# Kernel tuning notes

Hardware: AMD Instinct MI355X
Metric: run time of the kernel (lower is better)

## Reference

```python
import jax, jax.numpy as jnp
import numpy as np

D_MODEL = 1024
N_HEADS = 16
HEAD_DIM = D_MODEL // N_HEADS


def setup_inputs() -> dict:
    key = jax.random.key(0)
    ks = jax.random.split(key, 5)
    s = 1.0 / np.sqrt(D_MODEL)
    return {
        "x": jax.random.normal(ks[0], (2, 2048, D_MODEL), dtype=jnp.float32),
        "w_qkv": jax.random.uniform(ks[1], (3 * D_MODEL, D_MODEL), jnp.float32, -s, s),
        "b_qkv": jax.random.uniform(ks[2], (3 * D_MODEL,), jnp.float32, -s, s),
        "w_out": jax.random.uniform(ks[3], (D_MODEL, D_MODEL), jnp.float32, -s, s),
        "b_out": jax.random.uniform(ks[4], (D_MODEL,), jnp.float32, -s, s),
    }


def _attn(x, w_qkv, b_qkv, w_out, b_out):
    bsz, seq_len, _ = x.shape
    qkv = jnp.einsum('bsd,ed->bse', x, w_qkv) + b_qkv  # [B,S,3D]
    q, k, v = jnp.split(qkv, 3, axis=-1)
    def heads(t):  # [B,S,D] -> [B,H,S,Dh]
        return t.reshape(bsz, seq_len, N_HEADS, HEAD_DIM).transpose(0, 2, 1, 3)
    q, k, v = heads(q), heads(k), heads(v)
    scores = jnp.einsum('bhqd,bhkd->bhqk', q, k) / np.sqrt(HEAD_DIM)
    mask = jnp.tril(jnp.ones((seq_len, seq_len), dtype=bool))
    scores = jnp.where(mask, scores, -jnp.inf)
    probs = jax.nn.softmax(scores, axis=-1)
    attn = jnp.einsum('bhqk,bhkd->bhqd', probs, v)
    attn = attn.transpose(0, 2, 1, 3).reshape(bsz, seq_len, D_MODEL)
    return jnp.einsum('bsd,ed->bse', attn, w_out) + b_out


def reference(x, w_qkv, b_qkv, w_out, b_out):
    return _attn(x, w_qkv, b_qkv, w_out, b_out)
```

## Files before the change

### kernel.cpp

```cpp
#include <hip/hip_runtime.h>
#include <hip/hip_bf16.h>
#include <stdint.h>

#define SEQ     2048
#define BATCH   2
#define NHEADS  16
#define HDIM    64
#define DMODEL  1024
#define N3      3072
#define D2      2048
#define MTOT    (BATCH*SEQ)

typedef __attribute__((ext_vector_type(4))) float f32x4;
typedef __attribute__((ext_vector_type(8))) short bf16x8;

static __device__ inline unsigned short f2bf(float f) {
    union { float f; unsigned u; } v; v.f = f;
    unsigned r = (v.u + 0x7fffu + ((v.u >> 16) & 1u)) >> 16;
    return (unsigned short)r;
}
static __device__ inline unsigned pk2bf(float a, float b) {
    union { __hip_bfloat162 h; unsigned u; } c;
    c.h = __float22bfloat162_rn(make_float2(a, b));
    return c.u;
}

#define GLDS(gp, lp) __builtin_amdgcn_global_load_lds( \
    (const __attribute__((address_space(1))) void*)(gp), \
    (__attribute__((address_space(3))) void*)(lp), 16, 0, 0)

__global__ void cast_all(const float* __restrict__ x,
                         const float* __restrict__ wqkv,
                         const float* __restrict__ wout,
                         unsigned short* __restrict__ xb,
                         unsigned short* __restrict__ wqkvb,
                         unsigned short* __restrict__ woutb) {
    long i4 = (long)(blockIdx.x * blockDim.x + threadIdx.x) * 4;
    const float* src; unsigned short* dst; long off;
    if (i4 < 4194304L)      { src = x;    dst = xb;    off = i4; }
    else if (i4 < 7340032L) { src = wqkv; dst = wqkvb; off = i4 - 4194304L; }
    else                    { src = wout; dst = woutb; off = i4 - 7340032L; }
    float4 v = *(const float4*)(src + off);
    union { uint2 u; ushort4 s; } pk;
    pk.u.x = pk2bf(v.x, v.y); pk.u.y = pk2bf(v.z, v.w);
    *(ushort4*)(dst + off) = pk.s;
}

__global__ __launch_bounds__(512, 1) void gemm_qkv(
    const unsigned short* __restrict__ A,
    const unsigned short* __restrict__ B,
    const float* __restrict__ bias,
    unsigned short* __restrict__ qk,
    unsigned short* __restrict__ vT)
{
    __shared__ __align__(16) unsigned short sA[2][256][64];
    __shared__ __align__(16) unsigned short sB[2][256][64];
    const int tid  = threadIdx.x;
    const int w    = tid >> 6, lane = tid & 63;
    const int quad = lane >> 4, l16 = lane & 15, l7 = l16 & 7;
    const int wm = w >> 2, wn = w & 3;
    const int bid = blockIdx.x;
    const int m0 = (bid & 15) << 8;
    const int n0 = (bid >> 4) << 8;

    f32x4 acc[8][4];
    const f32x4 zero = {0.f, 0.f, 0.f, 0.f};
    #pragma unroll
    for (int i = 0; i < 8; i++)
        #pragma unroll
        for (int j = 0; j < 4; j++) acc[i][j] = zero;

    const int rsel = tid >> 3;
    const int sgl  = (tid & 7) ^ (rsel & 7);
    const unsigned short* gA = A + (long)(m0 + rsel) * 1024 + sgl * 8;
    const unsigned short* gB = B + (long)(n0 + rsel) * 1024 + sgl * 8;

    #pragma unroll
    for (int j = 0; j < 4; j++) {
        GLDS(gA + (long)(64 * j) * 1024, &sA[0][64 * j + w * 8][0]);
        GLDS(gB + (long)(64 * j) * 1024, &sB[0][64 * j + w * 8][0]);
    }

    auto compute_tile = [&](const unsigned short (*A_)[64],
                            const unsigned short (*B_)[64]) {
        #pragma unroll
        for (int mh = 0; mh < 2; mh++) {
            bf16x8 af[4][2];
            #pragma unroll
            for (int mt2 = 0; mt2 < 4; mt2++)
                #pragma unroll
                for (int kk = 0; kk < 2; kk++)
                    af[mt2][kk] = *(const bf16x8*)(
                        &A_[wm * 128 + mh * 64 + mt2 * 16 + l16]
                           [(((kk << 2) + quad) ^ l7) * 8]);
            #pragma unroll
            for (int nh = 0; nh < 2; nh++) {
                bf16x8 bfr[2][2];
                #pragma unroll
                for (int nt2 = 0; nt2 < 2; nt2++)
                    #pragma unroll
                    for (int kk = 0; kk < 2; kk++)
                        bfr[nt2][kk] = *(const bf16x8*)(
                            &B_[wn * 64 + nh * 32 + nt2 * 16 + l16]
                               [(((kk << 2) + quad) ^ l7) * 8]);
                #pragma unroll
                for (int mt2 = 0; mt2 < 4; mt2++)
                    #pragma unroll
                    for (int nt2 = 0; nt2 < 2; nt2++)
                        #pragma unroll
                        for (int kk = 0; kk < 2; kk++)
                            acc[mh * 4 + mt2][nh * 2 + nt2] =
                                __builtin_amdgcn_mfma_f32_16x16x32_bf16(
                                    af[mt2][kk], bfr[nt2][kk],
                                    acc[mh * 4 + mt2][nh * 2 + nt2], 0, 0, 0);
            }
        }
    };

    for (int t = 0; t < 15; ++t) {
        const int nb = (t + 1) & 1, cb = t & 1;
        const long ko = (long)(t + 1) * 64;
        #pragma unroll
        for (int j = 0; j < 4; j++) {
            GLDS(gA + (long)(64 * j) * 1024 + ko, &sA[nb][64 * j + w * 8][0]);
            GLDS(gB + (long)(64 * j) * 1024 + ko, &sB[nb][64 * j + w * 8][0]);
        }
        __builtin_amdgcn_sched_barrier(0);
        asm volatile("s_waitcnt vmcnt(8)" ::: "memory");
        __builtin_amdgcn_sched_barrier(0);
        __builtin_amdgcn_s_barrier();
        compute_tile(sA[cb], sB[cb]);
        asm volatile("s_waitcnt lgkmcnt(0)" ::: "memory");
        __builtin_amdgcn_sched_barrier(0);
        __builtin_amdgcn_s_barrier();
    }
    asm volatile("s_waitcnt vmcnt(0)" ::: "memory");
    __builtin_amdgcn_sched_barrier(0);
    __builtin_amdgcn_s_barrier();
    compute_tile(sA[1], sB[1]);

    if (n0 < 2048) {
        #pragma unroll
        for (int nt = 0; nt < 4; nt++) {
            const int n_g = n0 + wn * 64 + nt * 16 + l16;
            const float bv = bias[n_g];
            #pragma unroll
            for (int mt = 0; mt < 8; mt++) {
                #pragma unroll
                for (int r = 0; r < 4; r++) {
                    const int m_g = m0 + wm * 128 + mt * 16 + quad * 4 + r;
                    qk[(long)m_g * D2 + n_g] = f2bf(acc[mt][nt][r] + bv);
                }
            }
        }
    } else {
        const int b = m0 >> 11;
        #pragma unroll
        for (int nt = 0; nt < 4; nt++) {
            const int n_g = n0 + wn * 64 + nt * 16 + l16;
            const int dm = n_g - 2048;
            const long vrow = (long)(((b << 4) + (dm >> 6)) << 6) + (dm & 63);
            const float bv = bias[n_g];
            #pragma unroll
            for (int mt = 0; mt < 8; mt++) {
                const int m_g = m0 + wm * 128 + mt * 16 + quad * 4;
                union { uint2 u; ushort4 s; } pk;
                pk.u.x = pk2bf(acc[mt][nt][0] + bv, acc[mt][nt][1] + bv);
                pk.u.y = pk2bf(acc[mt][nt][2] + bv, acc[mt][nt][3] + bv);
                *(ushort4*)(vT + vrow * D2 + (m_g & 2047)) = pk.s;
            }
        }
    }
}

__global__ __launch_bounds__(256, 2) void gemm_out(
    const unsigned short* __restrict__ A,
    const unsigned short* __restrict__ B,
    const float* __restrict__ bias,
    float* __restrict__ C)
{
    __shared__ __align__(16) unsigned short sA[2][128][64];
    __shared__ __align__(16) unsigned short sB[2][64][64];
    const int tid  = threadIdx.x;
    const int wave = tid >> 6, lane = tid & 63;
    const int quad = lane >> 4, l16 = lane & 15, l7 = l16 & 7;
    const int wm = wave >> 1, wn = wave & 1;
    const int m0 = blockIdx.x * 128, n0 = blockIdx.y * 64;

    f32x4 acc[4][2];
    const f32x4 zero = {0.f, 0.f, 0.f, 0.f};
    #pragma unroll
    for (int i = 0; i < 4; i++) { acc[i][0] = zero; acc[i][1] = zero; }

    const int rsel = tid >> 3;
    const int sgl  = (tid & 7) ^ (rsel & 7);
    const unsigned short* gA0 = A + (long)(m0 + rsel) * 1024 + sgl * 8;
    const unsigned short* gB0 = B + (long)(n0 + rsel) * 1024 + sgl * 8;

    #pragma unroll
    for (int i = 0; i < 4; i++)
        GLDS(gA0 + (long)(32 * i) * 1024, &sA[0][32 * i + wave * 8][0]);
    #pragma unroll
    for (int i = 0; i < 2; i++)
        GLDS(gB0 + (long)(32 * i) * 1024, &sB[0][32 * i + wave * 8][0]);

    int buf = 0;
    for (int k0 = 0; k0 < 1024; k0 += 64, buf ^= 1) {
        __syncthreads();
        if (k0 + 64 < 1024) {
            #pragma unroll
            for (int i = 0; i < 4; i++)
                GLDS(gA0 + (long)(32 * i) * 1024 + k0 + 64, &sA[buf ^ 1][32 * i + wave * 8][0]);
            #pragma unroll
            for (int i = 0; i < 2; i++)
                GLDS(gB0 + (long)(32 * i) * 1024 + k0 + 64, &sB[buf ^ 1][32 * i + wave * 8][0]);
        }
        #pragma unroll
        for (int ks = 0; ks < 2; ks++) {
            bf16x8 af[4], bfr[2];
            #pragma unroll
            for (int mt = 0; mt < 4; mt++)
                af[mt] = *(const bf16x8*)(&sA[buf][wm * 64 + mt * 16 + l16][((ks * 4 + quad) ^ l7) * 8]);
            #pragma unroll
            for (int nt = 0; nt < 2; nt++)
                bfr[nt] = *(const bf16x8*)(&sB[buf][wn * 32 + nt * 16 + l16][((ks * 4 + quad) ^ l7) * 8]);
            #pragma unroll
            for (int mt = 0; mt < 4; mt++)
                #pragma unroll
                for (int nt = 0; nt < 2; nt++)
                    acc[mt][nt] = __builtin_amdgcn_mfma_f32_16x16x32_bf16(
                        af[mt], bfr[nt], acc[mt][nt], 0, 0, 0);
        }
    }
    #pragma unroll
    for (int nt = 0; nt < 2; nt++) {
        const int n_g = n0 + wn * 32 + nt * 16 + l16;
        const float bv = bias[n_g];
        #pragma unroll
        for (int mt = 0; mt < 4; mt++) {
            #pragma unroll
            for (int r = 0; r < 4; r++) {
                const int m_g = m0 + wm * 64 + mt * 16 + quad * 4 + r;
                C[(long)m_g * DMODEL + n_g] = acc[mt][nt][r] + bv;
            }
        }
    }
}

__global__ __launch_bounds__(512, 1) void attn_kernel(
    const unsigned short* __restrict__ qk,
    const unsigned short* __restrict__ vT,
    unsigned short* __restrict__ attn)
{
    __shared__ __align__(16) unsigned short sK [2][2][64][64];
    __shared__ __align__(16) unsigned short sVt[2][2][64][64];
    __shared__ __align__(16) unsigned short sP [8][16][64];

    const int tid  = threadIdx.x;
    const int w    = tid >> 6, lane = tid & 63;
    const int quad = lane >> 4, l16 = lane & 15, l7 = l16 & 7;

    const int bh = blockIdx.x;
    const int b  = bh >> 4, h = bh & 15;
    const int pair = blockIdx.y;
    const long rowb = (long)b * SEQ;

    const int rl = lane >> 3;
    const int sm = (lane & 7) ^ rl;
    const unsigned short* kg = qk + (rowb + w * 8 + rl) * D2 + 1024 + h * HDIM + sm * 8;
    const unsigned short* vg = vT + (long)(bh * 64 + w * 8 + rl) * D2 + sm * 8;

    const int s0 = quad ^ l7;
    const float C2 = 0.18033688011112042f;
    const f32x4 zero = {0.f, 0.f, 0.f, 0.f};

    #pragma unroll
    for (int ph = 0; ph < 2; ph++) {
        const int qtile  = ph ? (15 - pair) : pair;
        const int qbase  = qtile * 128;
        const int ntiles = 2 * qtile + 2;
        const int npairs = ntiles >> 1;

        bf16x8 qf0, qf1;
        {
            const unsigned short* qp = qk + (rowb + qbase + w * 16 + l16) * D2 + h * HDIM;
            qf0 = *(const bf16x8*)(qp + quad * 8);
            qf1 = *(const bf16x8*)(qp + 32 + quad * 8);
        }
        f32x4 Oacc[4];
        #pragma unroll
        for (int mf = 0; mf < 4; mf++) Oacc[mf] = zero;
        float l_i = 0.f;

        __syncthreads();
        {
            GLDS(kg,            &sK [0][0][w * 8][0]);
            GLDS(vg,            &sVt[0][0][w * 8][0]);
            GLDS(kg + 64L * D2, &sK [0][1][w * 8][0]);
            GLDS(vg + 64,       &sVt[0][1][w * 8][0]);
        }

        int buf = 0;
        for (int p = 0; p < npairs; p++, buf ^= 1) {
            __syncthreads();
            if (p + 1 < npairs) {
                const long o0 = (long)(2 * p + 2) * 64;
                const long o1 = (long)(2 * p + 3) * 64;
                GLDS(kg + o0 * D2, &sK [buf ^ 1][0][w * 8][0]);
                GLDS(vg + o0,      &sVt[buf ^ 1][0][w * 8][0]);
                GLDS(kg + o1 * D2, &sK [buf ^ 1][1][w * 8][0]);
                GLDS(vg + o1,      &sVt[buf ^ 1][1][w * 8][0]);
            }
            #pragma unroll
            for (int s = 0; s < 2; s++) {
                const int t = 2 * p + s;

                f32x4 st[4];
                __builtin_amdgcn_s_setprio(1);
                #pragma unroll
                for (int kvf = 0; kvf < 4; kvf++) {
                    bf16x8 kf0 = *(const bf16x8*)(&sK[buf][s][kvf * 16 + l16][s0 * 8]);
                    bf16x8 kf1 = *(const bf16x8*)(&sK[buf][s][kvf * 16 + l16][(s0 ^ 4) * 8]);
                    st[kvf] = __builtin_amdgcn_mfma_f32_16x16x32_bf16(kf0, qf0, zero, 0, 0, 0);
                    st[kvf] = __builtin_amdgcn_mfma_f32_16x16x32_bf16(kf1, qf1, st[kvf], 0, 0, 0);
                }
                __builtin_amdgcn_s_setprio(0);
                if (t >= 2 * qtile) {
                    const int ql = w * 16 + l16;
                    const int tb = (t - 2 * qtile) * 64;
                    #pragma unroll
                    for (int kvf = 0; kvf < 4; kvf++) {
                        const int kv = tb + kvf * 16 + quad * 4;
                        #pragma unroll
                        for (int r = 0; r < 4; r++)
                            if (kv + r > ql) st[kvf][r] = -1e30f;
                    }
                }
                #pragma unroll
                for (int kvf = 0; kvf < 4; kvf++) {
                    #pragma unroll
                    for (int r = 0; r < 4; r++)
                        st[kvf][r] = __builtin_amdgcn_exp2f(st[kvf][r] * C2);
                }
                f32x4 ps = (st[0] + st[1]) + (st[2] + st[3]);
                l_i += (ps[0] + ps[1]) + (ps[2] + ps[3]);

                #pragma unroll
                for (int kvf = 0; kvf < 4; kvf++) {
                    union { uint2 u; ushort4 s4; } pk;
                    pk.u.x = pk2bf(st[kvf][0], st[kvf][1]);
                    pk.u.y = pk2bf(st[kvf][2], st[kvf][3]);
                    const int seg = (kvf * 2 + (quad >> 1)) ^ l7;
                    *(ushort4*)(&sP[w][l16][seg * 8 + (quad & 1) * 4]) = pk.s4;
                }
                bf16x8 pf0 = *(const bf16x8*)(&sP[w][l16][(quad ^ l7) * 8]);
                bf16x8 pf1 = *(const bf16x8*)(&sP[w][l16][((4 + quad) ^ l7) * 8]);
                __builtin_amdgcn_s_setprio(1);
                #pragma unroll
                for (int mf = 0; mf < 4; mf++) {
                    bf16x8 vf0 = *(const bf16x8*)(&sVt[buf][s][mf * 16 + l16][s0 * 8]);
                    bf16x8 vf1 = *(const bf16x8*)(&sVt[buf][s][mf * 16 + l16][(s0 ^ 4) * 8]);
                    Oacc[mf] = __builtin_amdgcn_mfma_f32_16x16x32_bf16(vf0, pf0, Oacc[mf], 0, 0, 0);
                    Oacc[mf] = __builtin_amdgcn_mfma_f32_16x16x32_bf16(vf1, pf1, Oacc[mf], 0, 0, 0);
                }
                __builtin_amdgcn_s_setprio(0);
            }
        }
        float L = l_i;
        L += __shfl_xor(L, 16);
        L += __shfl_xor(L, 32);
        const float inv = 1.0f / L;
        const int q = qbase + w * 16 + l16;
        unsigned short* op = attn + (rowb + q) * DMODEL + h * HDIM + quad * 4;
        #pragma unroll
        for (int mf = 0; mf < 4; mf++) {
            union { uint2 u; ushort4 s4; } pk;
            pk.u.x = pk2bf(Oacc[mf][0] * inv, Oacc[mf][1] * inv);
            pk.u.y = pk2bf(Oacc[mf][2] * inv, Oacc[mf][3] * inv);
            *(ushort4*)(op + mf * 16) = pk.s4;
        }
    }
}

extern "C" void kernel_launch(void* const* d_in, const int* in_sizes, int n_in,
                              void* d_out, int out_size, void* d_ws, size_t ws_size,
                              hipStream_t stream) {
    const float* x    = (const float*)d_in[0];
    const float* wqkv = (const float*)d_in[1];
    const float* bqkv = (const float*)d_in[2];
    const float* wout = (const float*)d_in[3];
    const float* bout = (const float*)d_in[4];

    char* ws = (char*)d_ws;
    unsigned short* xb    = (unsigned short*)(ws);
    unsigned short* wqkvb = (unsigned short*)(ws + (8L << 20));
    unsigned short* woutb = (unsigned short*)(ws + (14L << 20));
    unsigned short* qkb   = (unsigned short*)(ws + (16L << 20));
    unsigned short* vTb   = (unsigned short*)(ws + (32L << 20));
    unsigned short* attnb = (unsigned short*)(ws + (40L << 20));

    cast_all<<<8192, 256, 0, stream>>>(x, wqkv, wout, xb, wqkvb, woutb);

    gemm_qkv<<<192, 512, 0, stream>>>(xb, wqkvb, bqkv, qkb, vTb);

    dim3 g2(32, 8);
    attn_kernel<<<g2, 512, 0, stream>>>(qkb, vTb, attnb);

    dim3 g3(32, 16);
    gemm_out<<<g3, 256, 0, stream>>>(attnb, woutb, bout, (float*)d_out);
}
```

Baseline: 174.2 us.

## Interleave QKV GEMM tile staging with quadrant MFMA phases and raise priority

```diff
diff --git a/kernel.cpp b/kernel.cpp
--- a/kernel.cpp
+++ b/kernel.cpp
@@ -74,99 +74,159 @@
     const int sgl  = (tid & 7) ^ (rsel & 7);
     const unsigned short* gA = A + (long)(m0 + rsel) * 1024 + sgl * 8;
     const unsigned short* gB = B + (long)(n0 + rsel) * 1024 + sgl * 8;
-
-    #pragma unroll
-    for (int j = 0; j < 4; j++) {
-        GLDS(gA + (long)(64 * j) * 1024, &sA[0][64 * j + w * 8][0]);
-        GLDS(gB + (long)(64 * j) * 1024, &sB[0][64 * j + w * 8][0]);
-    }
-
-    auto compute_tile = [&](const unsigned short (*A_)[64],
-                            const unsigned short (*B_)[64]) {
-        #pragma unroll
-        for (int mh = 0; mh < 2; mh++) {
-            bf16x8 af[4][2];
-            #pragma unroll
-            for (int mt2 = 0; mt2 < 4; mt2++)
+    const int srow = w * 8;
+
+    bf16x8 af[4][2];
+    bf16x8 bfr[2][2][2];
+
+    auto stageA = [&](int nb, int h, long ko) {
+        GLDS(gA + (long)(h * 128)      * 1024 + ko, &sA[nb][h * 128 +      srow][0]);
+        GLDS(gA + (long)(h * 128 + 64) * 1024 + ko, &sA[nb][h * 128 + 64 + srow][0]);
+    };
+    auto stageB = [&](int nb, int h, long ko) {
+        GLDS(gB + (long)(h * 128)      * 1024 + ko, &sB[nb][h * 128 +      srow][0]);
+        GLDS(gB + (long)(h * 128 + 64) * 1024 + ko, &sB[nb][h * 128 + 64 + srow][0]);
+    };
+    auto loadA = [&](int c, int mh) {
+        #pragma unroll
+        for (int mt2 = 0; mt2 < 4; mt2++)
+            #pragma unroll
+            for (int kk = 0; kk < 2; kk++)
+                af[mt2][kk] = *(const bf16x8*)(
+                    &sA[c][mh * 128 + wm * 64 + mt2 * 16 + l16]
+                          [(((kk << 2) + quad) ^ l7) * 8]);
+    };
+    auto loadB = [&](int c, int nh) {
+        #pragma unroll
+        for (int nt2 = 0; nt2 < 2; nt2++)
+            #pragma unroll
+            for (int kk = 0; kk < 2; kk++)
+                bfr[nh][nt2][kk] = *(const bf16x8*)(
+                    &sB[c][nh * 128 + wn * 32 + nt2 * 16 + l16]
+                          [(((kk << 2) + quad) ^ l7) * 8]);
+    };
+    auto mfmaQ = [&](int mh, int nh) {
+        __builtin_amdgcn_s_setprio(1);
+        #pragma unroll
+        for (int mt2 = 0; mt2 < 4; mt2++)
+            #pragma unroll
+            for (int nt2 = 0; nt2 < 2; nt2++)
                 #pragma unroll
                 for (int kk = 0; kk < 2; kk++)
-                    af[mt2][kk] = *(const bf16x8*)(
-                        &A_[wm * 128 + mh * 64 + mt2 * 16 + l16]
-                           [(((kk << 2) + quad) ^ l7) * 8]);
-            #pragma unroll
-            for (int nh = 0; nh < 2; nh++) {
-                bf16x8 bfr[2][2];
-                #pragma unroll
-                for (int nt2 = 0; nt2 < 2; nt2++)
-                    #pragma unroll
-                    for (int kk = 0; kk < 2; kk++)
-                        bfr[nt2][kk] = *(const bf16x8*)(
-                            &B_[wn * 64 + nh * 32 + nt2 * 16 + l16]
-                               [(((kk << 2) + quad) ^ l7) * 8]);
-                #pragma unroll
-                for (int mt2 = 0; mt2 < 4; mt2++)
-                    #pragma unroll
-                    for (int nt2 = 0; nt2 < 2; nt2++)
-                        #pragma unroll
-                        for (int kk = 0; kk < 2; kk++)
-                            acc[mh * 4 + mt2][nh * 2 + nt2] =
-                                __builtin_amdgcn_mfma_f32_16x16x32_bf16(
-                                    af[mt2][kk], bfr[nt2][kk],
-                                    acc[mh * 4 + mt2][nh * 2 + nt2], 0, 0, 0);
-            }
-        }
+                    acc[mh * 4 + mt2][nh * 2 + nt2] =
+                        __builtin_amdgcn_mfma_f32_16x16x32_bf16(
+                            af[mt2][kk], bfr[nh][nt2][kk],
+                            acc[mh * 4 + mt2][nh * 2 + nt2], 0, 0, 0);
+        __builtin_amdgcn_s_setprio(0);
     };
 
-    for (int t = 0; t < 15; ++t) {
-        const int nb = (t + 1) & 1, cb = t & 1;
-        const long ko = (long)(t + 1) * 64;
-        #pragma unroll
-        for (int j = 0; j < 4; j++) {
-            GLDS(gA + (long)(64 * j) * 1024 + ko, &sA[nb][64 * j + w * 8][0]);
-            GLDS(gB + (long)(64 * j) * 1024 + ko, &sB[nb][64 * j + w * 8][0]);
-        }
-        __builtin_amdgcn_sched_barrier(0);
-        asm volatile("s_waitcnt vmcnt(8)" ::: "memory");
-        __builtin_amdgcn_sched_barrier(0);
-        __builtin_amdgcn_s_barrier();
-        compute_tile(sA[cb], sB[cb]);
-        asm volatile("s_waitcnt lgkmcnt(0)" ::: "memory");
-        __builtin_amdgcn_sched_barrier(0);
-        __builtin_amdgcn_s_barrier();
-    }
-    asm volatile("s_waitcnt vmcnt(0)" ::: "memory");
+    stageB(0, 0, 0); stageB(0, 1, 0); stageA(0, 0, 0); stageA(0, 1, 0);
+    __builtin_amdgcn_sched_barrier(0);
+    asm volatile("s_waitcnt vmcnt(2)" ::: "memory");
     __builtin_amdgcn_sched_barrier(0);
     __builtin_amdgcn_s_barrier();
-    compute_tile(sA[1], sB[1]);
+
+    for (int t = 0; t < 15; ++t) {
+        const int c = t & 1, nb = c ^ 1;
+        const long ko = (long)(t + 1) * 64;
+
+        loadA(c, 0); loadB(c, 0);
+        stageB(nb, 0, ko);
+        __builtin_amdgcn_s_barrier();
+        asm volatile("s_waitcnt lgkmcnt(0)" ::: "memory");
+        __builtin_amdgcn_sched_barrier(0);
+        mfmaQ(0, 0);
+        __builtin_amdgcn_sched_barrier(0);
+        __builtin_amdgcn_s_barrier();
+
+        loadB(c, 1);
+        stageB(nb, 1, ko);
+        __builtin_amdgcn_sched_barrier(0);
+        asm volatile("s_waitcnt vmcnt(4)" ::: "memory");
+        __builtin_amdgcn_sched_barrier(0);
+        __builtin_amdgcn_s_barrier();
+        asm volatile("s_waitcnt lgkmcnt(0)" ::: "memory");
+        __builtin_amdgcn_sched_barrier(0);
+        mfmaQ(0, 1);
+        __builtin_amdgcn_sched_barrier(0);
+        __builtin_amdgcn_s_barrier();
+
+        loadA(c, 1);
+        stageA(nb, 0, ko);
+        __builtin_amdgcn_s_barrier();
+        asm volatile("s_waitcnt lgkmcnt(0)" ::: "memory");
+        __builtin_amdgcn_sched_barrier(0);
+        mfmaQ(1, 1);
+        __builtin_amdgcn_sched_barrier(0);
+        __builtin_amdgcn_s_barrier();
+
+        stageA(nb, 1, ko);
+        __builtin_amdgcn_sched_barrier(0);
+        asm volatile("s_waitcnt vmcnt(2)" ::: "memory");
+        __builtin_amdgcn_sched_barrier(0);
+        __builtin_amdgcn_s_barrier();
+        mfmaQ(1, 0);
+        __builtin_amdgcn_sched_barrier(0);
+        __builtin_amdgcn_s_barrier();
+    }
+    {
+        const int c = 1;
+        loadA(c, 0); loadB(c, 0);
+        __builtin_amdgcn_s_barrier();
+        asm volatile("s_waitcnt lgkmcnt(0)" ::: "memory");
+        __builtin_amdgcn_sched_barrier(0);
+        mfmaQ(0, 0);
+        __builtin_amdgcn_sched_barrier(0);
+        __builtin_amdgcn_s_barrier();
+
+        loadB(c, 1);
+        __builtin_amdgcn_sched_barrier(0);
+        asm volatile("s_waitcnt vmcnt(0)" ::: "memory");
+        __builtin_amdgcn_sched_barrier(0);
+        __builtin_amdgcn_s_barrier();
+        asm volatile("s_waitcnt lgkmcnt(0)" ::: "memory");
+        __builtin_amdgcn_sched_barrier(0);
+        mfmaQ(0, 1);
+        __builtin_amdgcn_sched_barrier(0);
+        __builtin_amdgcn_s_barrier();
+
+        loadA(c, 1);
+        __builtin_amdgcn_s_barrier();
+        asm volatile("s_waitcnt lgkmcnt(0)" ::: "memory");
+        __builtin_amdgcn_sched_barrier(0);
+        mfmaQ(1, 1);
+        mfmaQ(1, 0);
+    }
 
     if (n0 < 2048) {
         #pragma unroll
-        for (int nt = 0; nt < 4; nt++) {
-            const int n_g = n0 + wn * 64 + nt * 16 + l16;
+        for (int ni = 0; ni < 4; ni++) {
+            const int n_g = n0 + (ni >> 1) * 128 + wn * 32 + (ni & 1) * 16 + l16;
             const float bv = bias[n_g];
             #pragma unroll
-            for (int mt = 0; mt < 8; mt++) {
+            for (int mi = 0; mi < 8; mi++) {
+                const int mb = (mi >> 2) * 128 + wm * 64 + (mi & 3) * 16 + quad * 4;
                 #pragma unroll
                 for (int r = 0; r < 4; r++) {
-                    const int m_g = m0 + wm * 128 + mt * 16 + quad * 4 + r;
-                    qk[(long)m_g * D2 + n_g] = f2bf(acc[mt][nt][r] + bv);
+                    const int m_g = m0 + mb + r;
+                    qk[(long)m_g * D2 + n_g] = f2bf(acc[mi][ni][r] + bv);
                 }
             }
         }
     } else {
         const int b = m0 >> 11;
         #pragma unroll
-        for (int nt = 0; nt < 4; nt++) {
-            const int n_g = n0 + wn * 64 + nt * 16 + l16;
+        for (int ni = 0; ni < 4; ni++) {
+            const int n_g = n0 + (ni >> 1) * 128 + wn * 32 + (ni & 1) * 16 + l16;
             const int dm = n_g - 2048;
             const long vrow = (long)(((b << 4) + (dm >> 6)) << 6) + (dm & 63);
             const float bv = bias[n_g];
             #pragma unroll
-            for (int mt = 0; mt < 8; mt++) {
-                const int m_g = m0 + wm * 128 + mt * 16 + quad * 4;
+            for (int mi = 0; mi < 8; mi++) {
+                const int m_g = m0 + (mi >> 2) * 128 + wm * 64 + (mi & 3) * 16 + quad * 4;
                 union { uint2 u; ushort4 s; } pk;
-                pk.u.x = pk2bf(acc[mt][nt][0] + bv, acc[mt][nt][1] + bv);
-                pk.u.y = pk2bf(acc[mt][nt][2] + bv, acc[mt][nt][3] + bv);
+                pk.u.x = pk2bf(acc[mi][ni][0] + bv, acc[mi][ni][1] + bv);
+                pk.u.y = pk2bf(acc[mi][ni][2] + bv, acc[mi][ni][3] + bv);
                 *(ushort4*)(vT + vrow * D2 + (m_g & 2047)) = pk.s;
             }
         }
```

New measurement: 171.4 us. Within noise of the previous version (-1.6%).
